# Kernel tuning notes

Measured on AMD Instinct MI355X. Metric: run time of the kernel, lower is better.

Reference implementation:

```python
import jax, jax.numpy as jnp
import numpy as np

SYNC = 0.15
DEBATE = 0.15
N_FACTIONS = 8


def faction_sync_debate(h, step):
    # h: [Na, H] hidden rows of alive cells (contiguous, as gathered by alive_idx)
    n, H = h.shape
    n_f = min(N_FACTIONS, n // 2)
    if n_f < 2:
        return h
    fs = n // n_f
    hb = h[: n_f * fs].reshape(n_f, fs, H)
    fm = hb.mean(axis=1, keepdims=True)                  # faction means
    hb = (1.0 - SYNC) * hb + SYNC * fm                   # sync toward faction mean
    if step > 5:                                          # step is a static Python int
        # post-sync faction means equal pre-sync means; global opinion = mean of faction means
        go = hb.mean(axis=1).mean(axis=0)                # [H]
        dc = max(1, fs // 4)
        hb = hb.at[:, :dc].set((1.0 - DEBATE) * hb[:, :dc] + DEBATE * go)
    return jnp.concatenate([hb.reshape(n_f * fs, H), h[n_f * fs:]], axis=0)


def setup_inputs() -> dict:
    key = jax.random.key(0)
    ks = jax.random.split(key, 16)
    n_cells, n_alive = 262144, 131072
    in_d, hid, out_d = 64, 128, 64
    s = 0.1
    alive_idx = jnp.sort(jax.random.permutation(ks[14], n_cells)[:n_alive])
    return {
        "x": jax.random.normal(ks[0], (1, in_d), jnp.float32),
        "hiddens": jax.random.normal(ks[1], (n_cells, hid), jnp.float32) * 0.1,
        "Wa1": jax.random.normal(ks[2], (128, in_d + hid), jnp.float32) * s,
        "ba1": jax.random.normal(ks[3], (128,), jnp.float32) * s,
        "Wa2": jax.random.normal(ks[4], (out_d, 128), jnp.float32) * s,
        "ba2": jax.random.normal(ks[5], (out_d,), jnp.float32) * s,
        "Wg1": jax.random.normal(ks[6], (128, in_d + hid), jnp.float32) * s,
        "bg1": jax.random.normal(ks[7], (128,), jnp.float32) * s,
        "Wg2": jax.random.normal(ks[8], (out_d, 128), jnp.float32) * s,
        "bg2": jax.random.normal(ks[9], (out_d,), jnp.float32) * s,
        "W_ih": jax.random.normal(ks[10], (3 * hid, out_d + 1), jnp.float32) * s,
        "W_hh": jax.random.normal(ks[11], (3 * hid, hid), jnp.float32) * s,
        "b_ih": jax.random.normal(ks[12], (3 * hid,), jnp.float32) * s,
        "b_hh": jax.random.normal(ks[13], (3 * hid,), jnp.float32) * s,
        "alive_idx": alive_idx,
        "step": 10,
    }


def reference(x, hiddens, Wa1, ba1, Wa2, ba2, Wg1, bg1, Wg2, bg2,
              W_ih, W_hh, b_ih, b_hh, alive_idx, step):
    # Gather alive cells and run the tiny MLP+GRU for all of them at once
    h = hiddens[alive_idx]                                # [Na, H]
    xb = jnp.broadcast_to(x, (h.shape[0], x.shape[-1]))   # same x for every cell
    c = jnp.concatenate([xb, h], axis=-1)                 # [Na, in+H]
    a = jax.nn.relu(c @ Wa1.T + ba1) @ Wa2.T + ba2        # engine_a
    g = jax.nn.relu(c @ Wg1.T + bg1) @ Wg2.T + bg2        # engine_g
    out = a - g                                           # [Na, D]
    tension = jnp.mean(out * out, axis=-1, keepdims=True) # [Na, 1]
    # GRUCell (torch gate order r, z, n); mem_input is detached in the original
    mem_in = jax.lax.stop_gradient(jnp.concatenate([out, tension], axis=-1))
    gi = mem_in @ W_ih.T + b_ih                           # [Na, 3H]
    gh = h @ W_hh.T + b_hh                                # [Na, 3H]
    H = h.shape[-1]
    ir, iz, inn = gi[:, :H], gi[:, H:2 * H], gi[:, 2 * H:]
    hr, hz, hn = gh[:, :H], gh[:, H:2 * H], gh[:, 2 * H:]
    r = jax.nn.sigmoid(ir + hr)
    z = jax.nn.sigmoid(iz + hz)
    nn_ = jnp.tanh(inn + r * hn)
    new_h = jax.lax.stop_gradient((1.0 - z) * nn_ + z * h)  # detached in original
    new_h = faction_sync_debate(new_h, step)
    new_hiddens = hiddens.at[alive_idx].set(new_h)        # scatter-back state update
    # tension-softmax-weighted combination (weights detached via .item() in torch)
    t = tension[:, 0]
    w = jax.lax.stop_gradient(jax.nn.softmax(t, axis=0))
    combined = jnp.sum(w[:, None] * out, axis=0, keepdims=True)  # [1, D]
    mean_tension = jnp.mean(jax.lax.stop_gradient(t))
    return combined, mean_tension, new_hiddens
```

## Files before the change

kernel.cpp:

```cpp
#include <hip/hip_runtime.h>
#include <math.h>

#define TMC 64

typedef __attribute__((ext_vector_type(4))) float f32x4;
typedef __attribute__((ext_vector_type(8))) short bf16x8;

#define MFMA16(a,b,c) __builtin_amdgcn_mfma_f32_16x16x32_bf16((a),(b),(c),0,0,0)

__device__ __forceinline__ float sigmoidf_(float x){ return 1.0f/(1.0f + __expf(-x)); }
__device__ __forceinline__ float tanhf_(float x){
  float e = __expf(2.0f*x);
  return 1.0f - 2.0f/(e + 1.0f);
}

__device__ __forceinline__ unsigned short f2bf(float f){
  unsigned u = __float_as_uint(f);
  unsigned r = (u + 0x7FFFu + ((u>>16)&1u)) >> 16;
  return (unsigned short)r;
}
__device__ __forceinline__ unsigned pack2(float a, float b){
  return (unsigned)f2bf(a) | ((unsigned)f2bf(b)<<16);
}
__device__ __forceinline__ float bf2f(unsigned short u){ return __uint_as_float(((unsigned)u)<<16); }

__device__ __forceinline__ bf16x8 lds_ld8(const ushort* base, int byte){
  return *reinterpret_cast<const bf16x8*>(reinterpret_cast<const char*>(base) + byte);
}

__global__ void k_init(const float* __restrict__ x,
                       const float* __restrict__ Wa1, const float* __restrict__ ba1,
                       const float* __restrict__ Wg1, const float* __restrict__ bg1,
                       const float* __restrict__ Wa2, const float* __restrict__ Wg2,
                       const float* __restrict__ ba2, const float* __restrict__ bg2,
                       const float* __restrict__ Wih, const float* __restrict__ Whh,
                       const float* __restrict__ bih, const float* __restrict__ bhh,
                       const int* __restrict__ alive,
                       float* __restrict__ xab, float* __restrict__ b2d, float* __restrict__ brz,
                       ushort* __restrict__ W1f, ushort* __restrict__ W2f,
                       ushort* __restrict__ Wgf, ushort* __restrict__ Whf,
                       float* __restrict__ w64, int* __restrict__ iflg, int n){
  int tid = threadIdx.x;
  if (blockIdx.x == 0){
    __shared__ float sx[64];
    if (tid < 64) sx[tid] = x[tid];
    __syncthreads();
    if (tid < 128){
      const float* w = Wa1 + tid*192;
      float s = ba1[tid];
      #pragma unroll
      for (int i=0;i<64;i++) s += w[i]*sx[i];
      xab[tid] = s;
    } else {
      int j = tid-128;
      const float* w = Wg1 + j*192;
      float s = bg1[j];
      #pragma unroll
      for (int i=0;i<64;i++) s += w[i]*sx[i];
      xab[tid] = s;
    }
    if (tid < 64) b2d[tid] = ba2[tid] - bg2[tid];
    brz[tid] = bih[tid] + bhh[tid];
  }
  int stride = gridDim.x*blockDim.x;
  int t0 = blockIdx.x*blockDim.x + tid;
  for (int i=t0; i<256*128; i+=stride){
    int e=i&7, lane=(i>>3)&63, ks=(i>>9)&3, nt=i>>11;
    int r = nt*16 + (lane&15), k = ks*32 + (lane>>4)*8 + e;
    float v = (r<128) ? Wa1[r*192+64+k] : Wg1[(r-128)*192+64+k];
    W1f[i] = f2bf(v);
  }
  for (int i=t0; i<128*128; i+=stride){
    int e=i&7, lane=(i>>3)&63, ks=(i>>9)&3, nt=i>>11;
    int r = nt*16 + (lane&15), k = ks*32 + (lane>>4)*8 + e;
    float v = (r<64) ? Wa2[r*128+k] : Wg2[(r-64)*128+k];
    W2f[i] = f2bf(v);
  }
  for (int i=t0; i<384*64; i+=stride){
    int e=i&7, lane=(i>>3)&63, ks=(i>>9)&1, nt=i>>10;
    int r = nt*16 + (lane&15), k = ks*32 + (lane>>4)*8 + e;
    Wgf[i] = f2bf(Wih[r*65+k]);
  }
  for (int i=t0; i<384*128; i+=stride){
    int e=i&7, lane=(i>>3)&63, ks=(i>>9)&3, nt=i>>11;
    int r = nt*16 + (lane&15), k = ks*32 + (lane>>4)*8 + e;
    Whf[i] = f2bf(Whh[r*128+k]);
  }
  for (int i=t0; i<384; i+=stride) w64[i] = Wih[i*65+64];
  for (int i=t0; i<n; i+=stride) iflg[alive[i]] = i + 1;
}

__global__ __launch_bounds__(256,2) void k_main(
    const float* __restrict__ hiddens, const int* __restrict__ alive,
    const ushort* __restrict__ W1f, const ushort* __restrict__ W2f,
    const ushort* __restrict__ Wgf, const ushort* __restrict__ Whf,
    const float* __restrict__ w64,
    const float* __restrict__ xab, const float* __restrict__ b2d,
    const float* __restrict__ brz,
    const float* __restrict__ bih, const float* __restrict__ bhh,
    float* __restrict__ nh, float* __restrict__ facsum,
    float* __restrict__ recs, unsigned* __restrict__ tmax_u, float* __restrict__ tsum,
    int n, int fs, int nffs)
{
  __shared__ ushort sH[64*128];
  __shared__ __align__(16) ushort arena[64*256];
  __shared__ float sTS[4][64];
  __shared__ float sT[64];
  __shared__ float sE[64];
  __shared__ int   sIdx[TMC];

  ushort* sV1  = arena;
  ushort* sMIH = arena;

  int tid = threadIdx.x;
  int lane = tid & 63;
  int w = tid >> 6;
  int l15 = lane & 15;
  int lg  = lane >> 4;

  int base = blockIdx.x * TMC;
  int nvalid = n - base; if (nvalid > TMC) nvalid = TMC;

  if (tid < TMC){
    int t2 = tid < nvalid ? tid : (nvalid-1);
    sIdx[tid] = alive[base + t2];
  }
  __syncthreads();

  {
    int m = tid >> 2, c0 = (tid & 3) * 32;
    const float* src = hiddens + (size_t)sIdx[m]*128 + c0;
    #pragma unroll
    for (int j=0; j<32; j+=8){
      float4 v0 = *(const float4*)(src + j);
      float4 v1 = *(const float4*)(src + j + 4);
      uint4 pk;
      pk.x = pack2(v0.x, v0.y); pk.y = pack2(v0.z, v0.w);
      pk.z = pack2(v1.x, v1.y); pk.w = pack2(v1.z, v1.w);
      int byte = (m*256 + (c0 + j)*2) ^ ((m&7)<<4);
      *reinterpret_cast<uint4*>(reinterpret_cast<char*>(sH) + byte) = pk;
    }
  }
  __syncthreads();

  {
    int c0 = w*64;
    f32x4 acc[4][4];
    #pragma unroll
    for (int tm=0;tm<4;tm++)
      #pragma unroll
      for (int tn=0;tn<4;tn++) acc[tm][tn] = (f32x4)0.f;
    #pragma unroll
    for (int ks=0; ks<4; ks++){
      bf16x8 a[4], b[4];
      #pragma unroll
      for (int tm=0;tm<4;tm++){
        int row = tm*16 + l15;
        a[tm] = lds_ld8(sH, (row*256 + ks*64 + lg*16) ^ ((row&7)<<4));
      }
      #pragma unroll
      for (int tn=0;tn<4;tn++)
        b[tn] = *(const bf16x8*)(W1f + ((((w*4+tn)*4 + ks)*64 + lane)<<3));
      #pragma unroll
      for (int tm=0;tm<4;tm++)
        #pragma unroll
        for (int tn=0;tn<4;tn++)
          acc[tm][tn] = MFMA16(a[tm], b[tn], acc[tm][tn]);
    }
    #pragma unroll
    for (int tn=0;tn<4;tn++){
      int col = c0 + tn*16 + l15;
      float bias = xab[col];
      #pragma unroll
      for (int tm=0;tm<4;tm++){
        #pragma unroll
        for (int r=0;r<4;r++){
          int row = tm*16 + lg*4 + r;
          float v = fmaxf(acc[tm][tn][r] + bias, 0.f);
          int byte = (row*512 + col*2) ^ ((row&7)<<4);
          *(ushort*)((char*)sV1 + byte) = f2bf(v);
        }
      }
    }
  }
  __syncthreads();

  int jo2 = w*16;
  float outv[4][4];
  {
    f32x4 accA[4], accG[4];
    #pragma unroll
    for (int tm=0;tm<4;tm++){ accA[tm]=(f32x4)0.f; accG[tm]=(f32x4)0.f; }
    #pragma unroll
    for (int ks=0; ks<4; ks++){
      bf16x8 aA[4], aG[4], bA, bG;
      #pragma unroll
      for (int tm=0;tm<4;tm++){
        int row = tm*16 + l15;
        aA[tm] = lds_ld8(sV1, (row*512 + ks*64 + lg*16) ^ ((row&7)<<4));
        aG[tm] = lds_ld8(sV1, (row*512 + 256 + ks*64 + lg*16) ^ ((row&7)<<4));
      }
      bA = *(const bf16x8*)(W2f + (((w*4 + ks)*64 + lane)<<3));
      bG = *(const bf16x8*)(W2f + ((((4+w)*4 + ks)*64 + lane)<<3));
      #pragma unroll
      for (int tm=0;tm<4;tm++){
        accA[tm] = MFMA16(aA[tm], bA, accA[tm]);
        accG[tm] = MFMA16(aG[tm], bG, accG[tm]);
      }
    }
    int col = jo2 + l15;
    float bias = b2d[col];
    #pragma unroll
    for (int tm=0;tm<4;tm++)
      #pragma unroll
      for (int r=0;r<4;r++)
        outv[tm][r] = accA[tm][r] - accG[tm][r] + bias;
  }
  __syncthreads();

  {
    int col = jo2 + l15;
    float p[4][4];
    #pragma unroll
    for (int tm=0;tm<4;tm++){
      #pragma unroll
      for (int r=0;r<4;r++){
        int row = tm*16 + lg*4 + r;
        float o = outv[tm][r];
        int byte = (row*128 + col*2) ^ ((row&7)<<4);
        *(ushort*)((char*)sMIH + byte) = f2bf(o);
        p[tm][r] = o*o;
      }
    }
    #pragma unroll
    for (int off=1; off<16; off<<=1)
      #pragma unroll
      for (int tm=0;tm<4;tm++)
        #pragma unroll
        for (int r=0;r<4;r++) p[tm][r] += __shfl_xor(p[tm][r], off);
    if (l15 == 0){
      #pragma unroll
      for (int tm=0;tm<4;tm++)
        #pragma unroll
        for (int r=0;r<4;r++) sTS[w][tm*16 + lg*4 + r] = p[tm][r];
    }
  }
  __syncthreads();

  if (w == 0){
    int row = lane;
    float t = (sTS[0][row] + sTS[1][row] + sTS[2][row] + sTS[3][row]) * (1.0f/64.0f);
    sT[row] = t;
    bool valid = row < nvalid;
    float m2 = valid ? t : -1.f;
    #pragma unroll
    for (int off=1; off<64; off<<=1) m2 = fmaxf(m2, __shfl_xor(m2, off));
    float e  = valid ? __expf(t - m2) : 0.f;
    float st = valid ? t : 0.f;
    float se = e, ss = st;
    #pragma unroll
    for (int off=1; off<64; off<<=1){ se += __shfl_xor(se, off); ss += __shfl_xor(ss, off); }
    sE[row] = e;
    if (lane == 0){
      float* rec = recs + (size_t)blockIdx.x*66;
      rec[0] = m2; rec[1] = se;
      atomicMax(tmax_u, __float_as_uint(m2));
      atomicAdd(tsum, ss);
    }
  }
  __syncthreads();

  {
    float np = 0.f;
    #pragma unroll
    for (int tm=0;tm<4;tm++)
      #pragma unroll
      for (int r=0;r<4;r++)
        np += sE[tm*16 + lg*4 + r] * outv[tm][r];
    np += __shfl_xor(np, 16);
    np += __shfl_xor(np, 32);
    if (lg == 0) recs[(size_t)blockIdx.x*66 + 2 + jo2 + l15] = np;
  }

  float t16v[4][4];
  #pragma unroll
  for (int tm=0;tm<4;tm++)
    #pragma unroll
    for (int r=0;r<4;r++) t16v[tm][r] = sT[tm*16 + lg*4 + r];

  int lastrow = nvalid;
  if (base + lastrow > nffs) lastrow = nffs - base;
  int f0 = (fs > 0 && base < nffs) ? base / fs : 0;
  bool onefac = (lastrow <= 0) || ((base + lastrow - 1) / fs == f0);

  {
    int jo3 = w*32;
    int ntb = 2*w;
    f32x4 aR[4][2], aZ[4][2], aN[4][2], aI[4][2];
    #pragma unroll
    for (int tm=0;tm<4;tm++)
      #pragma unroll
      for (int tn=0;tn<2;tn++){
        aR[tm][tn]=(f32x4)0.f; aZ[tm][tn]=(f32x4)0.f;
        aN[tm][tn]=(f32x4)0.f; aI[tm][tn]=(f32x4)0.f;
      }

    #pragma unroll
    for (int ks=0; ks<4; ks++){
      bf16x8 a[4];
      #pragma unroll
      for (int tm=0;tm<4;tm++){
        int row = tm*16 + l15;
        a[tm] = lds_ld8(sH, (row*256 + ks*64 + lg*16) ^ ((row&7)<<4));
      }
      bf16x8 bR[2], bZ[2], bN[2];
      #pragma unroll
      for (int tn=0;tn<2;tn++){
        bR[tn] = *(const bf16x8*)(Whf + ((((     ntb+tn)*4 + ks)*64 + lane)<<3));
        bZ[tn] = *(const bf16x8*)(Whf + ((((8  + ntb+tn)*4 + ks)*64 + lane)<<3));
        bN[tn] = *(const bf16x8*)(Whf + ((((16 + ntb+tn)*4 + ks)*64 + lane)<<3));
      }
      #pragma unroll
      for (int tm=0;tm<4;tm++)
        #pragma unroll
        for (int tn=0;tn<2;tn++){
          aR[tm][tn] = MFMA16(a[tm], bR[tn], aR[tm][tn]);
          aZ[tm][tn] = MFMA16(a[tm], bZ[tn], aZ[tm][tn]);
          aN[tm][tn] = MFMA16(a[tm], bN[tn], aN[tm][tn]);
        }
    }
    #pragma unroll
    for (int ks=0; ks<2; ks++){
      bf16x8 a[4];
      #pragma unroll
      for (int tm=0;tm<4;tm++){
        int row = tm*16 + l15;
        a[tm] = lds_ld8(sMIH, (row*128 + ks*64 + lg*16) ^ ((row&7)<<4));
      }
      bf16x8 bR[2], bZ[2], bI[2];
      #pragma unroll
      for (int tn=0;tn<2;tn++){
        bR[tn] = *(const bf16x8*)(Wgf + ((((     ntb+tn)*2 + ks)*64 + lane)<<3));
        bZ[tn] = *(const bf16x8*)(Wgf + ((((8  + ntb+tn)*2 + ks)*64 + lane)<<3));
        bI[tn] = *(const bf16x8*)(Wgf + ((((16 + ntb+tn)*2 + ks)*64 + lane)<<3));
      }
      #pragma unroll
      for (int tm=0;tm<4;tm++)
        #pragma unroll
        for (int tn=0;tn<2;tn++){
          aR[tm][tn] = MFMA16(a[tm], bR[tn], aR[tm][tn]);
          aZ[tm][tn] = MFMA16(a[tm], bZ[tn], aZ[tm][tn]);
          aI[tm][tn] = MFMA16(a[tm], bI[tn], aI[tm][tn]);
        }
    }

    #pragma unroll
    for (int tn=0;tn<2;tn++){
      int col = jo3 + tn*16 + l15;
      float bR0 = brz[col],      wR = w64[col];
      float bZ0 = brz[128+col],  wZ = w64[128+col];
      float bI0 = bih[256+col],  wI = w64[256+col];
      float bN0 = bhh[256+col];
      float fsum = 0.f;
      #pragma unroll
      for (int tm=0;tm<4;tm++){
        #pragma unroll
        for (int r=0;r<4;r++){
          int row = tm*16 + lg*4 + r;
          float t = t16v[tm][r];
          float rr = sigmoidf_(aR[tm][tn][r] + bR0 + t*wR);
          float zz = sigmoidf_(aZ[tm][tn][r] + bZ0 + t*wZ);
          float nnv = tanhf_(aI[tm][tn][r] + bI0 + t*wI + rr*(aN[tm][tn][r] + bN0));
          int hb = (row*256 + col*2) ^ ((row&7)<<4);
          float hv = bf2f(*(const ushort*)((const char*)sH + hb));
          float v = (1.f - zz)*nnv + zz*hv;
          if (row < nvalid) nh[(size_t)sIdx[row]*128 + col] = v;
          if (onefac){
            if (row < lastrow) fsum += v;
          } else if (row < lastrow){
            atomicAdd(&facsum[((base+row)/fs)*128 + col], v);
          }
        }
      }
      if (onefac && lastrow > 0){
        fsum += __shfl_xor(fsum, 16);
        fsum += __shfl_xor(fsum, 32);
        if (lg == 0) atomicAdd(&facsum[f0*128 + col], fsum);
      }
    }
  }
}

__global__ void k_comb1(const float* __restrict__ recs, int nrec,
                        const unsigned* __restrict__ tmax_u,
                        float* __restrict__ num, float* __restrict__ S){
  int tid = threadIdx.x;
  int c = tid & 63, rg = tid >> 6;
  float M = __uint_as_float(*tmax_u);
  float acc = 0.f, sacc = 0.f;
  for (int r = blockIdx.x*4 + rg; r < nrec; r += gridDim.x*4){
    const float* rec = recs + (size_t)r*66;
    float e = __expf(rec[0] - M);
    acc += e * rec[2+c];
    if (c == 0) sacc += e * rec[1];
  }
  __shared__ float sn[4][64];
  __shared__ float ss[4];
  sn[rg][c] = acc;
  if (c == 0) ss[rg] = sacc;
  __syncthreads();
  if (tid < 64) atomicAdd(&num[tid], sn[0][tid]+sn[1][tid]+sn[2][tid]+sn[3][tid]);
  if (tid == 64) atomicAdd(S, ss[0]+ss[1]+ss[2]+ss[3]);
}

__global__ void k_final(const float* __restrict__ num, const float* __restrict__ S,
                        const float* __restrict__ tsum, const float* __restrict__ facsum,
                        float* __restrict__ out, float* __restrict__ go, float* __restrict__ fmn,
                        int n, int n_f, int fs){
  int tid = threadIdx.x;
  if (tid < 64) out[tid] = num[tid] / *S;
  else if (tid == 64) out[64] = *tsum / (float)n;
  if (tid >= 128 && n_f >= 2){
    int j = tid - 128;
    float s = 0.f;
    for (int f=0; f<n_f; f++){
      float v = facsum[f*128+j];
      s += v;
      fmn[f*128+j] = v / (float)fs;
    }
    go[j] = s / (float)(n_f*fs);
  }
}

__global__ void k_post(const float* __restrict__ hid, const int* __restrict__ iflags,
                       const float* __restrict__ fmn, const float* __restrict__ go,
                       const int* __restrict__ step_p,
                       float* __restrict__ nh, int fs, int dc, int nffs, int total){
  bool debate = (*step_p > 5);
  int stride = gridDim.x*blockDim.x;
  for (int idx = blockIdx.x*blockDim.x + threadIdx.x; idx < total; idx += stride){
    int c = idx >> 5, q = idx & 31, j0 = q*4;
    size_t off = (size_t)c*128 + j0;
    int fl = iflags[c];
    if (fl == 0){
      float4 h4 = *(const float4*)(hid + off);
      nh[off] = h4.x; nh[off+1] = h4.y; nh[off+2] = h4.z; nh[off+3] = h4.w;
    } else {
      int i = fl - 1;
      if (i < nffs){
        float v0 = nh[off], v1 = nh[off+1], v2 = nh[off+2], v3 = nh[off+3];
        int f = i / fs;
        float4 fm4 = *(const float4*)(fmn + f*128 + j0);
        v0 = 0.85f*v0 + 0.15f*fm4.x;
        v1 = 0.85f*v1 + 0.15f*fm4.y;
        v2 = 0.85f*v2 + 0.15f*fm4.z;
        v3 = 0.85f*v3 + 0.15f*fm4.w;
        if (debate && (i - f*fs) < dc){
          float4 g4 = *(const float4*)(go + j0);
          v0 = 0.85f*v0 + 0.15f*g4.x;
          v1 = 0.85f*v1 + 0.15f*g4.y;
          v2 = 0.85f*v2 + 0.15f*g4.z;
          v3 = 0.85f*v3 + 0.15f*g4.w;
        }
        nh[off] = v0; nh[off+1] = v1; nh[off+2] = v2; nh[off+3] = v3;
      }
    }
  }
}

extern "C" void kernel_launch(void* const* d_in, const int* in_sizes, int n_in,
                              void* d_out, int out_size, void* d_ws, size_t ws_size,
                              hipStream_t stream){
  const float* x    = (const float*)d_in[0];
  const float* hid  = (const float*)d_in[1];
  const float* Wa1  = (const float*)d_in[2];
  const float* ba1  = (const float*)d_in[3];
  const float* Wa2  = (const float*)d_in[4];
  const float* ba2  = (const float*)d_in[5];
  const float* Wg1  = (const float*)d_in[6];
  const float* bg1  = (const float*)d_in[7];
  const float* Wg2  = (const float*)d_in[8];
  const float* bg2  = (const float*)d_in[9];
  const float* Wih  = (const float*)d_in[10];
  const float* Whh  = (const float*)d_in[11];
  const float* bih  = (const float*)d_in[12];
  const float* bhh  = (const float*)d_in[13];
  const int*   alive= (const int*)d_in[14];
  const int*   step = (const int*)d_in[15];

  int n = in_sizes[14];
  int n_cells = in_sizes[1] / 128;
  int n_f = (n/2 < 8) ? n/2 : 8;
  int fs   = (n_f >= 2) ? n / n_f : 0;
  int nffs = (n_f >= 2) ? n_f * fs : 0;
  int dc   = (fs/4 > 1) ? fs/4 : 1;
  int nblocks = (n + TMC - 1) / TMC;

  float* out = (float*)d_out;
  float* nh  = out + 65;
  float* ws  = (float*)d_ws;

  float* xab   = ws + 0;
  float* b2d   = ws + 256;
  float* brz   = ws + 320;
  float* facs  = ws + 576;
  float* num   = ws + 1600;
  float* Ssum  = ws + 1664;
  float* tsum  = ws + 1665;
  unsigned* tmax_u = (unsigned*)(ws + 1666);
  float* go    = ws + 1668;
  float* fmn   = ws + 1796;
  float* w64   = ws + 2820;
  float* recs  = ws + 3204;
  int recs_end = 3204 + ((nblocks*66 + 3) & ~3);
  int* iflags  = (int*)(ws + recs_end);
  int woff = (recs_end + n_cells + 3) & ~3;
  ushort* W1f  = (ushort*)(ws + woff);
  ushort* W2f  = (ushort*)(ws + woff + 16384);
  ushort* Wgf  = (ushort*)(ws + woff + 24576);
  ushort* Whf  = (ushort*)(ws + woff + 36864);

  hipMemsetAsync(ws + 576, 0, 1092*sizeof(float), stream);
  hipMemsetAsync(iflags, 0, (size_t)n_cells*sizeof(int), stream);

  k_init<<<256,256,0,stream>>>(x, Wa1, ba1, Wg1, bg1, Wa2, Wg2, ba2, bg2,
                               Wih, Whh, bih, bhh, alive,
                               xab, b2d, brz, W1f, W2f, Wgf, Whf, w64, iflags, n);
  k_main<<<nblocks,256,0,stream>>>(hid, alive, W1f, W2f, Wgf, Whf, w64, xab, b2d, brz,
                                   bih, bhh, nh, facs, recs, tmax_u, tsum,
                                   n, fs, nffs);
  k_comb1<<<64,256,0,stream>>>(recs, nblocks, tmax_u, num, Ssum);
  k_final<<<1,256,0,stream>>>(num, Ssum, tsum, facs, out, go, fmn, n, n_f, fs);
  k_post<<<2048,256,0,stream>>>(hid, iflags, fmn, go, step, nh, fs, dc, nffs, n_cells*32);
}
```

Before: 186.7 us.

## Make each wave own 16 rows end-to-end, removing block-wide barriers

Restructures k_main so that each of the four waves processes its own 16 rows through all three GEMM stages (MLP layer 1, layer 2, GRU) using private LDS slices. Previously the waves split output columns across a shared 64-row tile, which needed several __syncthreads between stages. The softmax partials are now combined per wave and merged once at the end. The cost is that every wave now loads all of the weight B-fragments from global/L2 memory, roughly four times more weight traffic per block, and uses more accumulator registers per wave.

```diff
diff --git a/kernel.cpp b/kernel.cpp
--- a/kernel.cpp
+++ b/kernel.cpp
@@ -23,10 +23,6 @@
   return (unsigned)f2bf(a) | ((unsigned)f2bf(b)<<16);
 }
 __device__ __forceinline__ float bf2f(unsigned short u){ return __uint_as_float(((unsigned)u)<<16); }
-
-__device__ __forceinline__ bf16x8 lds_ld8(const ushort* base, int byte){
-  return *reinterpret_cast<const bf16x8*>(reinterpret_cast<const char*>(base) + byte);
-}
 
 __global__ void k_init(const float* __restrict__ x,
                        const float* __restrict__ Wa1, const float* __restrict__ ba1,
@@ -102,15 +98,11 @@
     float* __restrict__ recs, unsigned* __restrict__ tmax_u, float* __restrict__ tsum,
     int n, int fs, int nffs)
 {
-  __shared__ ushort sH[64*128];
-  __shared__ __align__(16) ushort arena[64*256];
-  __shared__ float sTS[4][64];
-  __shared__ float sT[64];
-  __shared__ float sE[64];
-  __shared__ int   sIdx[TMC];
-
-  ushort* sV1  = arena;
-  ushort* sMIH = arena;
+  __shared__ ushort sH[4*16*128];
+  __shared__ __align__(16) ushort arena[4*16*256];
+  __shared__ float sNp[4][64];
+  __shared__ float sM[4], sS[4], sS2[4];
+  __shared__ int   sIdx[64];
 
   int tid = threadIdx.x;
   int lane = tid & 63;
@@ -120,16 +112,22 @@
 
   int base = blockIdx.x * TMC;
   int nvalid = n - base; if (nvalid > TMC) nvalid = TMC;
-
-  if (tid < TMC){
-    int t2 = tid < nvalid ? tid : (nvalid-1);
-    sIdx[tid] = alive[base + t2];
-  }
-  __syncthreads();
+  int rbase = w*16;
+  int gbase = base + rbase;
+  int nvw = nvalid - rbase; if (nvw < 0) nvw = 0; if (nvw > 16) nvw = 16;
+
+  char* whb = (char*)sH    + w*4096;
+  char* wvb = (char*)arena + w*8192;
+
+  if (lane < 16){
+    int t2 = rbase + lane; if (t2 >= nvalid) t2 = nvalid - 1;
+    sIdx[rbase + lane] = alive[base + t2];
+  }
 
   {
-    int m = tid >> 2, c0 = (tid & 3) * 32;
-    const float* src = hiddens + (size_t)sIdx[m]*128 + c0;
+    int lr = lane >> 2, c0 = (lane & 3) * 32;
+    int idx = sIdx[rbase + lr];
+    const float* src = hiddens + (size_t)idx*128 + c0;
     #pragma unroll
     for (int j=0; j<32; j+=8){
       float4 v0 = *(const float4*)(src + j);
@@ -137,256 +135,207 @@
       uint4 pk;
       pk.x = pack2(v0.x, v0.y); pk.y = pack2(v0.z, v0.w);
       pk.z = pack2(v1.x, v1.y); pk.w = pack2(v1.z, v1.w);
-      int byte = (m*256 + (c0 + j)*2) ^ ((m&7)<<4);
-      *reinterpret_cast<uint4*>(reinterpret_cast<char*>(sH) + byte) = pk;
-    }
-  }
-  __syncthreads();
+      int byte = (lr*256 + (c0 + j)*2) ^ ((lr&7)<<4);
+      *reinterpret_cast<uint4*>(whb + byte) = pk;
+    }
+  }
 
   {
-    int c0 = w*64;
-    f32x4 acc[4][4];
-    #pragma unroll
-    for (int tm=0;tm<4;tm++)
-      #pragma unroll
-      for (int tn=0;tn<4;tn++) acc[tm][tn] = (f32x4)0.f;
+    f32x4 acc1[16];
+    #pragma unroll
+    for (int tn=0;tn<16;tn++) acc1[tn] = (f32x4)0.f;
     #pragma unroll
     for (int ks=0; ks<4; ks++){
-      bf16x8 a[4], b[4];
-      #pragma unroll
-      for (int tm=0;tm<4;tm++){
-        int row = tm*16 + l15;
-        a[tm] = lds_ld8(sH, (row*256 + ks*64 + lg*16) ^ ((row&7)<<4));
-      }
-      #pragma unroll
-      for (int tn=0;tn<4;tn++)
-        b[tn] = *(const bf16x8*)(W1f + ((((w*4+tn)*4 + ks)*64 + lane)<<3));
-      #pragma unroll
-      for (int tm=0;tm<4;tm++)
-        #pragma unroll
-        for (int tn=0;tn<4;tn++)
-          acc[tm][tn] = MFMA16(a[tm], b[tn], acc[tm][tn]);
-    }
-    #pragma unroll
-    for (int tn=0;tn<4;tn++){
-      int col = c0 + tn*16 + l15;
+      bf16x8 a = *reinterpret_cast<const bf16x8*>(whb + ((l15*256 + ks*64 + lg*16) ^ ((l15&7)<<4)));
+      #pragma unroll
+      for (int tn=0;tn<16;tn++){
+        bf16x8 b = *(const bf16x8*)(W1f + (((tn*4 + ks)*64 + lane)<<3));
+        acc1[tn] = MFMA16(a, b, acc1[tn]);
+      }
+    }
+    #pragma unroll
+    for (int tn=0;tn<16;tn++){
+      int col = tn*16 + l15;
       float bias = xab[col];
       #pragma unroll
-      for (int tm=0;tm<4;tm++){
-        #pragma unroll
-        for (int r=0;r<4;r++){
-          int row = tm*16 + lg*4 + r;
-          float v = fmaxf(acc[tm][tn][r] + bias, 0.f);
-          int byte = (row*512 + col*2) ^ ((row&7)<<4);
-          *(ushort*)((char*)sV1 + byte) = f2bf(v);
-        }
-      }
-    }
-  }
-  __syncthreads();
-
-  int jo2 = w*16;
+      for (int r=0;r<4;r++){
+        int lr = lg*4 + r;
+        float v = fmaxf(acc1[tn][r] + bias, 0.f);
+        int byte = (lr*512 + col*2) ^ ((lr&7)<<4);
+        *(ushort*)(wvb + byte) = f2bf(v);
+      }
+    }
+  }
+
   float outv[4][4];
   {
     f32x4 accA[4], accG[4];
     #pragma unroll
-    for (int tm=0;tm<4;tm++){ accA[tm]=(f32x4)0.f; accG[tm]=(f32x4)0.f; }
+    for (int tn=0;tn<4;tn++){ accA[tn]=(f32x4)0.f; accG[tn]=(f32x4)0.f; }
     #pragma unroll
     for (int ks=0; ks<4; ks++){
-      bf16x8 aA[4], aG[4], bA, bG;
-      #pragma unroll
-      for (int tm=0;tm<4;tm++){
-        int row = tm*16 + l15;
-        aA[tm] = lds_ld8(sV1, (row*512 + ks*64 + lg*16) ^ ((row&7)<<4));
-        aG[tm] = lds_ld8(sV1, (row*512 + 256 + ks*64 + lg*16) ^ ((row&7)<<4));
-      }
-      bA = *(const bf16x8*)(W2f + (((w*4 + ks)*64 + lane)<<3));
-      bG = *(const bf16x8*)(W2f + ((((4+w)*4 + ks)*64 + lane)<<3));
-      #pragma unroll
-      for (int tm=0;tm<4;tm++){
-        accA[tm] = MFMA16(aA[tm], bA, accA[tm]);
-        accG[tm] = MFMA16(aG[tm], bG, accG[tm]);
-      }
-    }
-    int col = jo2 + l15;
-    float bias = b2d[col];
-    #pragma unroll
-    for (int tm=0;tm<4;tm++)
+      bf16x8 aA = *reinterpret_cast<const bf16x8*>(wvb + ((l15*512 +       ks*64 + lg*16) ^ ((l15&7)<<4)));
+      bf16x8 aG = *reinterpret_cast<const bf16x8*>(wvb + ((l15*512 + 256 + ks*64 + lg*16) ^ ((l15&7)<<4)));
+      #pragma unroll
+      for (int tn=0;tn<4;tn++){
+        bf16x8 bA = *(const bf16x8*)(W2f + ((( tn     *4 + ks)*64 + lane)<<3));
+        bf16x8 bG = *(const bf16x8*)(W2f + ((((4+tn)  *4 + ks)*64 + lane)<<3));
+        accA[tn] = MFMA16(aA, bA, accA[tn]);
+        accG[tn] = MFMA16(aG, bG, accG[tn]);
+      }
+    }
+    #pragma unroll
+    for (int tn=0;tn<4;tn++){
+      int col = tn*16 + l15;
+      float bias = b2d[col];
       #pragma unroll
       for (int r=0;r<4;r++)
-        outv[tm][r] = accA[tm][r] - accG[tm][r] + bias;
-  }
-  __syncthreads();
-
+        outv[tn][r] = accA[tn][r] - accG[tn][r] + bias;
+    }
+  }
+
+  #pragma unroll
+  for (int tn=0;tn<4;tn++){
+    int col = tn*16 + l15;
+    #pragma unroll
+    for (int r=0;r<4;r++){
+      int lr = lg*4 + r;
+      int byte = (lr*128 + col*2) ^ ((lr&7)<<4);
+      *(ushort*)(wvb + byte) = f2bf(outv[tn][r]);
+    }
+  }
+
+  float t16v[4];
   {
-    int col = jo2 + l15;
-    float p[4][4];
-    #pragma unroll
-    for (int tm=0;tm<4;tm++){
-      #pragma unroll
-      for (int r=0;r<4;r++){
-        int row = tm*16 + lg*4 + r;
-        float o = outv[tm][r];
-        int byte = (row*128 + col*2) ^ ((row&7)<<4);
-        *(ushort*)((char*)sMIH + byte) = f2bf(o);
-        p[tm][r] = o*o;
-      }
+    float p[4];
+    #pragma unroll
+    for (int r=0;r<4;r++){
+      float s = 0.f;
+      #pragma unroll
+      for (int tn=0;tn<4;tn++) s += outv[tn][r]*outv[tn][r];
+      p[r] = s;
     }
     #pragma unroll
     for (int off=1; off<16; off<<=1)
       #pragma unroll
-      for (int tm=0;tm<4;tm++)
-        #pragma unroll
-        for (int r=0;r<4;r++) p[tm][r] += __shfl_xor(p[tm][r], off);
-    if (l15 == 0){
-      #pragma unroll
-      for (int tm=0;tm<4;tm++)
-        #pragma unroll
-        for (int r=0;r<4;r++) sTS[w][tm*16 + lg*4 + r] = p[tm][r];
-    }
-  }
-  __syncthreads();
-
-  if (w == 0){
-    int row = lane;
-    float t = (sTS[0][row] + sTS[1][row] + sTS[2][row] + sTS[3][row]) * (1.0f/64.0f);
-    sT[row] = t;
-    bool valid = row < nvalid;
-    float m2 = valid ? t : -1.f;
-    #pragma unroll
-    for (int off=1; off<64; off<<=1) m2 = fmaxf(m2, __shfl_xor(m2, off));
-    float e  = valid ? __expf(t - m2) : 0.f;
-    float st = valid ? t : 0.f;
-    float se = e, ss = st;
-    #pragma unroll
-    for (int off=1; off<64; off<<=1){ se += __shfl_xor(se, off); ss += __shfl_xor(ss, off); }
-    sE[row] = e;
-    if (lane == 0){
-      float* rec = recs + (size_t)blockIdx.x*66;
-      rec[0] = m2; rec[1] = se;
-      atomicMax(tmax_u, __float_as_uint(m2));
-      atomicAdd(tsum, ss);
-    }
-  }
-  __syncthreads();
+      for (int r=0;r<4;r++) p[r] += __shfl_xor(p[r], off);
+    float mw = -1.f, se = 0.f, st = 0.f;
+    float ev[4];
+    #pragma unroll
+    for (int r=0;r<4;r++){
+      float t = p[r] * (1.0f/64.0f);
+      t16v[r] = t;
+      bool valid = (lg*4 + r) < nvw;
+      mw = fmaxf(mw, valid ? t : -1.f);
+    }
+    mw = fmaxf(mw, __shfl_xor(mw, 16));
+    mw = fmaxf(mw, __shfl_xor(mw, 32));
+    #pragma unroll
+    for (int r=0;r<4;r++){
+      bool valid = (lg*4 + r) < nvw;
+      ev[r] = valid ? __expf(t16v[r] - mw) : 0.f;
+      se += ev[r];
+      st += valid ? t16v[r] : 0.f;
+    }
+    se += __shfl_xor(se, 16); se += __shfl_xor(se, 32);
+    st += __shfl_xor(st, 16); st += __shfl_xor(st, 32);
+    if (lane == 0){ sM[w] = mw; sS[w] = se; sS2[w] = st; }
+    #pragma unroll
+    for (int tn=0;tn<4;tn++){
+      float np = 0.f;
+      #pragma unroll
+      for (int r=0;r<4;r++) np += ev[r] * outv[tn][r];
+      np += __shfl_xor(np, 16);
+      np += __shfl_xor(np, 32);
+      if (lg == 0) sNp[w][tn*16 + l15] = np;
+    }
+  }
 
   {
-    float np = 0.f;
-    #pragma unroll
-    for (int tm=0;tm<4;tm++)
-      #pragma unroll
-      for (int r=0;r<4;r++)
-        np += sE[tm*16 + lg*4 + r] * outv[tm][r];
-    np += __shfl_xor(np, 16);
-    np += __shfl_xor(np, 32);
-    if (lg == 0) recs[(size_t)blockIdx.x*66 + 2 + jo2 + l15] = np;
-  }
-
-  float t16v[4][4];
-  #pragma unroll
-  for (int tm=0;tm<4;tm++)
-    #pragma unroll
-    for (int r=0;r<4;r++) t16v[tm][r] = sT[tm*16 + lg*4 + r];
-
-  int lastrow = nvalid;
-  if (base + lastrow > nffs) lastrow = nffs - base;
-  int f0 = (fs > 0 && base < nffs) ? base / fs : 0;
-  bool onefac = (lastrow <= 0) || ((base + lastrow - 1) / fs == f0);
-
-  {
-    int jo3 = w*32;
-    int ntb = 2*w;
-    f32x4 aR[4][2], aZ[4][2], aN[4][2], aI[4][2];
-    #pragma unroll
-    for (int tm=0;tm<4;tm++)
-      #pragma unroll
-      for (int tn=0;tn<2;tn++){
-        aR[tm][tn]=(f32x4)0.f; aZ[tm][tn]=(f32x4)0.f;
-        aN[tm][tn]=(f32x4)0.f; aI[tm][tn]=(f32x4)0.f;
-      }
-
+    f32x4 aR[8], aZ[8], aN[8], aI[8];
+    #pragma unroll
+    for (int tn=0;tn<8;tn++){
+      aR[tn]=(f32x4)0.f; aZ[tn]=(f32x4)0.f; aN[tn]=(f32x4)0.f; aI[tn]=(f32x4)0.f;
+    }
     #pragma unroll
     for (int ks=0; ks<4; ks++){
-      bf16x8 a[4];
-      #pragma unroll
-      for (int tm=0;tm<4;tm++){
-        int row = tm*16 + l15;
-        a[tm] = lds_ld8(sH, (row*256 + ks*64 + lg*16) ^ ((row&7)<<4));
-      }
-      bf16x8 bR[2], bZ[2], bN[2];
-      #pragma unroll
-      for (int tn=0;tn<2;tn++){
-        bR[tn] = *(const bf16x8*)(Whf + ((((     ntb+tn)*4 + ks)*64 + lane)<<3));
-        bZ[tn] = *(const bf16x8*)(Whf + ((((8  + ntb+tn)*4 + ks)*64 + lane)<<3));
-        bN[tn] = *(const bf16x8*)(Whf + ((((16 + ntb+tn)*4 + ks)*64 + lane)<<3));
-      }
-      #pragma unroll
-      for (int tm=0;tm<4;tm++)
-        #pragma unroll
-        for (int tn=0;tn<2;tn++){
-          aR[tm][tn] = MFMA16(a[tm], bR[tn], aR[tm][tn]);
-          aZ[tm][tn] = MFMA16(a[tm], bZ[tn], aZ[tm][tn]);
-          aN[tm][tn] = MFMA16(a[tm], bN[tn], aN[tm][tn]);
-        }
+      bf16x8 a = *reinterpret_cast<const bf16x8*>(whb + ((l15*256 + ks*64 + lg*16) ^ ((l15&7)<<4)));
+      #pragma unroll
+      for (int tn=0;tn<8;tn++){
+        bf16x8 bR = *(const bf16x8*)(Whf + ((((     tn)*4 + ks)*64 + lane)<<3));
+        bf16x8 bZ = *(const bf16x8*)(Whf + ((((8  + tn)*4 + ks)*64 + lane)<<3));
+        bf16x8 bN = *(const bf16x8*)(Whf + ((((16 + tn)*4 + ks)*64 + lane)<<3));
+        aR[tn] = MFMA16(a, bR, aR[tn]);
+        aZ[tn] = MFMA16(a, bZ, aZ[tn]);
+        aN[tn] = MFMA16(a, bN, aN[tn]);
+      }
     }
     #pragma unroll
     for (int ks=0; ks<2; ks++){
-      bf16x8 a[4];
-      #pragma unroll
-      for (int tm=0;tm<4;tm++){
-        int row = tm*16 + l15;
-        a[tm] = lds_ld8(sMIH, (row*128 + ks*64 + lg*16) ^ ((row&7)<<4));
-      }
-      bf16x8 bR[2], bZ[2], bI[2];
-      #pragma unroll
-      for (int tn=0;tn<2;tn++){
-        bR[tn] = *(const bf16x8*)(Wgf + ((((     ntb+tn)*2 + ks)*64 + lane)<<3));
-        bZ[tn] = *(const bf16x8*)(Wgf + ((((8  + ntb+tn)*2 + ks)*64 + lane)<<3));
-        bI[tn] = *(const bf16x8*)(Wgf + ((((16 + ntb+tn)*2 + ks)*64 + lane)<<3));
-      }
-      #pragma unroll
-      for (int tm=0;tm<4;tm++)
-        #pragma unroll
-        for (int tn=0;tn<2;tn++){
-          aR[tm][tn] = MFMA16(a[tm], bR[tn], aR[tm][tn]);
-          aZ[tm][tn] = MFMA16(a[tm], bZ[tn], aZ[tm][tn]);
-          aI[tm][tn] = MFMA16(a[tm], bI[tn], aI[tm][tn]);
-        }
-    }
-
-    #pragma unroll
-    for (int tn=0;tn<2;tn++){
-      int col = jo3 + tn*16 + l15;
+      bf16x8 a = *reinterpret_cast<const bf16x8*>(wvb + ((l15*128 + ks*64 + lg*16) ^ ((l15&7)<<4)));
+      #pragma unroll
+      for (int tn=0;tn<8;tn++){
+        bf16x8 bR = *(const bf16x8*)(Wgf + ((((     tn)*2 + ks)*64 + lane)<<3));
+        bf16x8 bZ = *(const bf16x8*)(Wgf + ((((8  + tn)*2 + ks)*64 + lane)<<3));
+        bf16x8 bI = *(const bf16x8*)(Wgf + ((((16 + tn)*2 + ks)*64 + lane)<<3));
+        aR[tn] = MFMA16(a, bR, aR[tn]);
+        aZ[tn] = MFMA16(a, bZ, aZ[tn]);
+        aI[tn] = MFMA16(a, bI, aI[tn]);
+      }
+    }
+
+    int last = nvw;
+    if (gbase + last > nffs) last = nffs - gbase;
+    if (last < 0) last = 0;
+    int f0 = (fs > 0 && gbase < nffs) ? gbase / fs : 0;
+    bool onefac = (last <= 0) || ((gbase + last - 1) / fs == f0);
+
+    #pragma unroll
+    for (int tn=0;tn<8;tn++){
+      int col = tn*16 + l15;
       float bR0 = brz[col],      wR = w64[col];
       float bZ0 = brz[128+col],  wZ = w64[128+col];
       float bI0 = bih[256+col],  wI = w64[256+col];
       float bN0 = bhh[256+col];
       float fsum = 0.f;
       #pragma unroll
-      for (int tm=0;tm<4;tm++){
-        #pragma unroll
-        for (int r=0;r<4;r++){
-          int row = tm*16 + lg*4 + r;
-          float t = t16v[tm][r];
-          float rr = sigmoidf_(aR[tm][tn][r] + bR0 + t*wR);
-          float zz = sigmoidf_(aZ[tm][tn][r] + bZ0 + t*wZ);
-          float nnv = tanhf_(aI[tm][tn][r] + bI0 + t*wI + rr*(aN[tm][tn][r] + bN0));
-          int hb = (row*256 + col*2) ^ ((row&7)<<4);
-          float hv = bf2f(*(const ushort*)((const char*)sH + hb));
-          float v = (1.f - zz)*nnv + zz*hv;
-          if (row < nvalid) nh[(size_t)sIdx[row]*128 + col] = v;
-          if (onefac){
-            if (row < lastrow) fsum += v;
-          } else if (row < lastrow){
-            atomicAdd(&facsum[((base+row)/fs)*128 + col], v);
-          }
+      for (int r=0;r<4;r++){
+        int lr = lg*4 + r;
+        float t = t16v[r];
+        float rr = sigmoidf_(aR[tn][r] + bR0 + t*wR);
+        float zz = sigmoidf_(aZ[tn][r] + bZ0 + t*wZ);
+        float nnv = tanhf_(aI[tn][r] + bI0 + t*wI + rr*(aN[tn][r] + bN0));
+        int hb = (lr*256 + col*2) ^ ((lr&7)<<4);
+        float hv = bf2f(*(const ushort*)(whb + hb));
+        float v = (1.f - zz)*nnv + zz*hv;
+        if (lr < nvw) nh[(size_t)sIdx[rbase+lr]*128 + col] = v;
+        if (onefac){
+          if (lr < last) fsum += v;
+        } else if (lr < last){
+          atomicAdd(&facsum[((gbase+lr)/fs)*128 + col], v);
         }
       }
-      if (onefac && lastrow > 0){
+      if (onefac && last > 0){
         fsum += __shfl_xor(fsum, 16);
         fsum += __shfl_xor(fsum, 32);
         if (lg == 0) atomicAdd(&facsum[f0*128 + col], fsum);
       }
+    }
+  }
+
+  __syncthreads();
+  if (w == 0){
+    float m0 = sM[0], m1 = sM[1], m2v = sM[2], m3 = sM[3];
+    float Mb = fmaxf(fmaxf(m0,m1), fmaxf(m2v,m3));
+    float e0 = __expf(m0-Mb), e1 = __expf(m1-Mb), e2 = __expf(m2v-Mb), e3 = __expf(m3-Mb);
+    float nb = e0*sNp[0][lane] + e1*sNp[1][lane] + e2*sNp[2][lane] + e3*sNp[3][lane];
+    float* rec = recs + (size_t)blockIdx.x*66;
+    rec[2+lane] = nb;
+    if (lane == 0){
+      rec[0] = Mb;
+      rec[1] = e0*sS[0] + e1*sS[1] + e2*sS[2] + e3*sS[3];
+      atomicMax(tmax_u, __float_as_uint(Mb));
+      atomicAdd(tsum, sS2[0]+sS2[1]+sS2[2]+sS2[3]);
     }
   }
 }
```

Result: slower. 280.2 us (+50.1%).
